# Kernel optimization log

Hardware: AMD Instinct MI355X
Metric: run time of the kernel (lower is better)

The kernel has to match this reference:

```python
import jax, jax.numpy as jnp
import numpy as np

N, E, IN_C, HID_C, OUT_C = 50000, 800000, 64, 64, 8
NEG_SLOPE = 0.2


def setup_inputs() -> dict:
    key = jax.random.key(0)
    ks = jax.random.split(key, 12)
    return {
        "x": jax.random.normal(ks[0], (N, IN_C), dtype=jnp.float32),
        "edge_index": jax.random.randint(ks[1], (2, E), 0, N, dtype=jnp.int64),
        "edge_value": jax.random.uniform(ks[2], (E,), dtype=jnp.float32),
        "W1": jax.random.normal(ks[3], (IN_C, HID_C), dtype=jnp.float32) * 0.1,
        "a1_src": jax.random.normal(ks[4], (HID_C,), dtype=jnp.float32) * 0.1,
        "a1_dst": jax.random.normal(ks[5], (HID_C,), dtype=jnp.float32) * 0.1,
        "b1": jnp.zeros((HID_C,), dtype=jnp.float32),
        "W2": jax.random.normal(ks[6], (HID_C, OUT_C), dtype=jnp.float32) * 0.1,
        "a2_src": jax.random.normal(ks[7], (OUT_C,), dtype=jnp.float32) * 0.1,
        "a2_dst": jax.random.normal(ks[8], (OUT_C,), dtype=jnp.float32) * 0.1,
        "b2": jnp.zeros((OUT_C,), dtype=jnp.float32),
    }


def _rgat_conv(x, src, dst, edge_value, W, a_src, a_dst, b, n_nodes):
    # Linear transform: [N, out_c]
    h = x @ W
    # Per-node attention halves, gathered per edge -> per-edge logit
    e_src = h @ a_src  # [N]
    e_dst = h @ a_dst  # [N]
    logits = jax.nn.leaky_relu(e_src[src] + e_dst[dst], negative_slope=NEG_SLOPE)  # [E]
    # Segment softmax over destination neighborhoods (numerically stable)
    m = jax.ops.segment_max(logits, dst, num_segments=n_nodes)  # [N]
    ex = jnp.exp(logits - m[dst])
    denom = jax.ops.segment_sum(ex, dst, num_segments=n_nodes)  # [N]
    alpha = ex / (denom[dst] + 1e-16)  # [E]
    # Edge-weighted messages, scatter-aggregate to destinations
    msg = (alpha * edge_value)[:, None] * h[src]  # [E, out_c]
    out = jax.ops.segment_sum(msg, dst, num_segments=n_nodes)  # [N, out_c]
    return out + b


def reference(x, edge_index, edge_value, W1, a1_src, a1_dst, b1, W2, a2_src, a2_dst, b2):
    src, dst = edge_index[0], edge_index[1]
    n = x.shape[0]
    hid = _rgat_conv(x, src, dst, edge_value, W1, a1_src, a1_dst, b1, n)
    hid = jax.nn.relu(hid)
    out = _rgat_conv(hid, src, dst, edge_value, W2, a2_src, a2_dst, b2, n)
    return jax.nn.log_softmax(out, axis=1)
```

## Files before the change

### kernel.cpp

```cpp
#include <hip/hip_runtime.h>
#include <hip/hip_fp16.h>
#include <math.h>


#define CHUNK 4096
#define NBKT  256
#define CAP   6144

typedef unsigned long long ull;
typedef float v2f __attribute__((ext_vector_type(2)));

struct PartSmem {
    int lhist[NBKT], lbase[NBKT], lcur[NBKT], gbase[NBKT];
    ull buf[CHUNK];
};
struct GemmSmem {
    float4 Wl[64 * 16];
    float  Xt[64 * 64];
};
union FusedSmem { PartSmem p; GemmSmem g; };


__global__ void __launch_bounds__(256) part_gemm_kernel(
    const int* __restrict__ src, const int* __restrict__ dst,
    const float* __restrict__ ev, int* __restrict__ bcnt,
    ull* __restrict__ ped, int E, int nchunks,
    const float* __restrict__ x, const float* __restrict__ W,
    const float* __restrict__ a_src, const float* __restrict__ a_dst,
    unsigned* __restrict__ h, float* __restrict__ es, float* __restrict__ ed,
    int N)
{
    __shared__ FusedSmem sm;
    const int t = threadIdx.x;

    if (blockIdx.x < nchunks) {
        int e0 = blockIdx.x * CHUNK;
        int cnt = min(CHUNK, E - e0);
        sm.p.lhist[t] = 0;
        __syncthreads();
        for (int i = t; i < cnt; i += 256)
            atomicAdd(&sm.p.lhist[dst[e0 + i] >> 8], 1);
        __syncthreads();
        int myc = sm.p.lhist[t];
        sm.p.lbase[t] = myc;
        __syncthreads();
        for (int o = 1; o < 256; o <<= 1) {
            int add = (t >= o) ? sm.p.lbase[t - o] : 0;
            __syncthreads();
            sm.p.lbase[t] += add;
            __syncthreads();
        }
        int excl = sm.p.lbase[t] - myc;
        sm.p.gbase[t] = myc ? atomicAdd(&bcnt[t], myc) : 0;
        __syncthreads();
        sm.p.lbase[t] = excl;
        sm.p.lcur[t] = excl;
        __syncthreads();
        for (int i = t; i < cnt; i += 256) {
            int e = e0 + i;
            int d = dst[e];
            int b = d >> 8;
            unsigned p = (unsigned)src[e] | ((unsigned)(d & 255) << 16)
                       | ((unsigned)b << 24);
            ull q = (ull)p | ((ull)__float_as_uint(ev[e]) << 32);
            int r = atomicAdd(&sm.p.lcur[b], 1);
            sm.p.buf[r] = q;
        }
        __syncthreads();
        for (int i = t; i < cnt; i += 256) {
            ull q = sm.p.buf[i];
            int b = (int)((q >> 24) & 255);
            ped[(size_t)b * CAP + sm.p.gbase[b] + i - sm.p.lbase[b]] = q;
        }
        return;
    }

    const int n0 = (blockIdx.x - nchunks) * 64;

    #pragma unroll
    for (int i = 0; i < 4; ++i)
        sm.g.Wl[t + i * 256] = ((const float4*)W)[t + i * 256];

    #pragma unroll
    for (int i = 0; i < 4; ++i) {
        int f   = t + i * 256;
        int row = f >> 4, kq = f & 15;
        int grow = n0 + row;
        float4 v = make_float4(0.f, 0.f, 0.f, 0.f);
        if (grow < N) v = ((const float4*)x)[(size_t)grow * 16 + kq];
        int rs = row ^ ((kq & 3) << 2);
        sm.g.Xt[(kq * 4 + 0) * 64 + rs] = v.x;
        sm.g.Xt[(kq * 4 + 1) * 64 + rs] = v.y;
        sm.g.Xt[(kq * 4 + 2) * 64 + rs] = v.z;
        sm.g.Xt[(kq * 4 + 3) * 64 + rs] = v.w;
    }

    const int tx = t & 15;
    const int ty = t >> 4;
    const float4 asv = ((const float4*)a_src)[tx];
    const float4 adv = ((const float4*)a_dst)[tx];
    __syncthreads();

    float4 acc0 = make_float4(0.f,0.f,0.f,0.f);
    float4 acc1 = make_float4(0.f,0.f,0.f,0.f);
    float4 acc2 = make_float4(0.f,0.f,0.f,0.f);
    float4 acc3 = make_float4(0.f,0.f,0.f,0.f);

    #pragma unroll 8
    for (int k = 0; k < 64; ++k) {
        int swz = (k >> 2) & 3;
        const float4 xr = *(const float4*)&sm.g.Xt[k * 64 + ((ty ^ swz) << 2)];
        const float4 wv = sm.g.Wl[k * 16 + tx];
        acc0.x += xr.x * wv.x; acc0.y += xr.x * wv.y;
        acc0.z += xr.x * wv.z; acc0.w += xr.x * wv.w;
        acc1.x += xr.y * wv.x; acc1.y += xr.y * wv.y;
        acc1.z += xr.y * wv.z; acc1.w += xr.y * wv.w;
        acc2.x += xr.z * wv.x; acc2.y += xr.z * wv.y;
        acc2.z += xr.z * wv.z; acc2.w += xr.z * wv.w;
        acc3.x += xr.w * wv.x; acc3.y += xr.w * wv.y;
        acc3.z += xr.w * wv.z; acc3.w += xr.w * wv.w;
    }

    float4 accs[4] = {acc0, acc1, acc2, acc3};
    #pragma unroll
    for (int r = 0; r < 4; ++r) {
        int grow = n0 + ty * 4 + r;
        float4 a = accs[r];
        if (grow < N) {
            int lo = __builtin_amdgcn_cvt_pk_fp8_f32(a.x, a.y, 0, false);
            int pk = __builtin_amdgcn_cvt_pk_fp8_f32(a.z, a.w, lo, true);
            h[(size_t)grow * 16 + tx] = (unsigned)pk;
        }
        float ps = a.x * asv.x + a.y * asv.y + a.z * asv.z + a.w * asv.w;
        float pd = a.x * adv.x + a.y * adv.y + a.z * adv.z + a.w * adv.w;
        #pragma unroll
        for (int o = 8; o > 0; o >>= 1) {
            ps += __shfl_xor(ps, o);
            pd += __shfl_xor(pd, o);
        }
        if (tx == 0 && grow < N) { es[grow] = ps; ed[grow] = pd; }
    }
}


__global__ void __launch_bounds__(1024) csrw_agg64_kernel(
    const ull* __restrict__ ped, const int* __restrict__ bcnt,
    const float* __restrict__ es1, const float* __restrict__ ed1,
    int* __restrict__ off, int* __restrict__ deg, ull* __restrict__ csre,
    const unsigned* __restrict__ h1, const float* __restrict__ b1,
    const float* __restrict__ W2, const float* __restrict__ a2s,
    const float* __restrict__ a2d, float* __restrict__ h2,
    float* __restrict__ es2, float* __restrict__ ed2, int N)
{
    __shared__ int    lhist[256], lbase[256], lcur[256], degl[256];
    __shared__ float  den1[256], eds[256];
    __shared__ float  W2s[64 * 8];
    __shared__ float  w1v[CAP];
    __shared__ unsigned short svl[CAP];

    const int b = blockIdx.x, t = threadIdx.x;
    const int cnt = min(bcnt[b], CAP);
    const size_t base = (size_t)b * CAP;

    if (t < 256) {
        const int nodeT = b * 256 + t;
        lhist[t] = 0;
        den1[t] = 0.f;
        eds[t] = (nodeT < N) ? ed1[nodeT] : 0.f;
    }
    if (t < 128) ((float4*)W2s)[t] = ((const float4*)W2)[t];
    __syncthreads();

    for (int i = t; i < cnt; i += 1024)
        atomicAdd(&lhist[(int)((ped[base + i] >> 16) & 255)], 1);
    __syncthreads();
    int myc = (t < 256) ? lhist[t] : 0;
    if (t < 256) lbase[t] = myc;
    __syncthreads();
    for (int o = 1; o < 256; o <<= 1) {
        int add = (t >= o && t < 256) ? lbase[t - o] : 0;
        __syncthreads();
        if (t < 256) lbase[t] += add;
        __syncthreads();
    }
    if (t < 256) {
        const int excl = lbase[t] - myc;
        const int nodeT = b * 256 + t;
        lcur[t] = excl;
        degl[t] = myc;
        if (nodeT < N) { off[nodeT] = (int)base + excl; deg[nodeT] = myc; }
    }
    __syncthreads();
    if (t < 256) lbase[t] -= myc;
    __syncthreads();

    for (int i = t; i < cnt; i += 1024) {
        const ull q = ped[base + i];
        const int sv   = (int)(q & 0xFFFFull);
        const int dloc = (int)((q >> 16) & 255);
        const float evv = __uint_as_float((unsigned)(q >> 32));
        float z = es1[sv] + eds[dloc];
        float l = z > 0.f ? z : 0.2f * z;
        float e = __expf(l);
        atomicAdd(&den1[dloc], e);
        const int pos = atomicAdd(&lcur[dloc], 1);
        w1v[pos] = e * evv;
        svl[pos] = (unsigned short)sv;
        csre[base + pos] = (q & 0xFFFFFFFF00000000ull)
                         | ((ull)(unsigned)(dloc << 16)) | (ull)(unsigned)sv;
    }
    __syncthreads();

    const int wid = t >> 6, lane = t & 63;
    const int grp = lane >> 2, sl = lane & 3;
    const int nloc = wid * 16 + grp;
    const int n = b * 256 + nloc;
    if (n >= N) return;

    const int dg   = degl[nloc];
    const int lbeg = lbase[nloc];

    float acc[16];
    #pragma unroll
    for (int k = 0; k < 16; ++k) acc[k] = 0.f;

    for (int j0 = 0; j0 < dg; j0 += 4) {
        #pragma unroll
        for (int ts = 0; ts < 4; ++ts) {
            const int jj  = j0 + ts;
            const int idx = lbeg + min(jj, dg - 1);
            const int svt = (int)svl[idx];
            float wt = w1v[idx];
            wt = (jj < dg) ? wt : 0.f;
            const uint4 u = *(const uint4*)&h1[(size_t)svt * 16 + sl * 4];
            v2f fa = __builtin_amdgcn_cvt_pk_f32_fp8((int)u.x, false);
            v2f fb = __builtin_amdgcn_cvt_pk_f32_fp8((int)u.x, true);
            v2f fc = __builtin_amdgcn_cvt_pk_f32_fp8((int)u.y, false);
            v2f fd = __builtin_amdgcn_cvt_pk_f32_fp8((int)u.y, true);
            v2f fe = __builtin_amdgcn_cvt_pk_f32_fp8((int)u.z, false);
            v2f ff = __builtin_amdgcn_cvt_pk_f32_fp8((int)u.z, true);
            v2f fg = __builtin_amdgcn_cvt_pk_f32_fp8((int)u.w, false);
            v2f fh = __builtin_amdgcn_cvt_pk_f32_fp8((int)u.w, true);
            acc[0]  += wt * fa.x; acc[1]  += wt * fa.y;
            acc[2]  += wt * fb.x; acc[3]  += wt * fb.y;
            acc[4]  += wt * fc.x; acc[5]  += wt * fc.y;
            acc[6]  += wt * fd.x; acc[7]  += wt * fd.y;
            acc[8]  += wt * fe.x; acc[9]  += wt * fe.y;
            acc[10] += wt * ff.x; acc[11] += wt * ff.y;
            acc[12] += wt * fg.x; acc[13] += wt * fg.y;
            acc[14] += wt * fh.x; acc[15] += wt * fh.y;
        }
    }

    const float inv = 1.f / (den1[nloc] + 1e-16f);

    const float4 b1v0 = *(const float4*)&b1[sl * 16];
    const float4 b1v1 = *(const float4*)&b1[sl * 16 + 4];
    const float4 b1v2 = *(const float4*)&b1[sl * 16 + 8];
    const float4 b1v3 = *(const float4*)&b1[sl * 16 + 12];

    float hid[16];
    hid[0]  = fmaxf(acc[0]  * inv + b1v0.x, 0.f);
    hid[1]  = fmaxf(acc[1]  * inv + b1v0.y, 0.f);
    hid[2]  = fmaxf(acc[2]  * inv + b1v0.z, 0.f);
    hid[3]  = fmaxf(acc[3]  * inv + b1v0.w, 0.f);
    hid[4]  = fmaxf(acc[4]  * inv + b1v1.x, 0.f);
    hid[5]  = fmaxf(acc[5]  * inv + b1v1.y, 0.f);
    hid[6]  = fmaxf(acc[6]  * inv + b1v1.z, 0.f);
    hid[7]  = fmaxf(acc[7]  * inv + b1v1.w, 0.f);
    hid[8]  = fmaxf(acc[8]  * inv + b1v2.x, 0.f);
    hid[9]  = fmaxf(acc[9]  * inv + b1v2.y, 0.f);
    hid[10] = fmaxf(acc[10] * inv + b1v2.z, 0.f);
    hid[11] = fmaxf(acc[11] * inv + b1v2.w, 0.f);
    hid[12] = fmaxf(acc[12] * inv + b1v3.x, 0.f);
    hid[13] = fmaxf(acc[13] * inv + b1v3.y, 0.f);
    hid[14] = fmaxf(acc[14] * inv + b1v3.z, 0.f);
    hid[15] = fmaxf(acc[15] * inv + b1v3.w, 0.f);

    float p[8];
    #pragma unroll
    for (int o = 0; o < 8; ++o) p[o] = 0.f;
    #pragma unroll
    for (int k = 0; k < 16; ++k) {
        const float4 wA = *(const float4*)&W2s[(sl * 16 + k) * 8];
        const float4 wB = *(const float4*)&W2s[(sl * 16 + k) * 8 + 4];
        p[0] += hid[k] * wA.x; p[1] += hid[k] * wA.y;
        p[2] += hid[k] * wA.z; p[3] += hid[k] * wA.w;
        p[4] += hid[k] * wB.x; p[5] += hid[k] * wB.y;
        p[6] += hid[k] * wB.z; p[7] += hid[k] * wB.w;
    }
    float s4[4];
    {
        const bool hi = (sl & 1);
        #pragma unroll
        for (int k = 0; k < 4; ++k) {
            float keep = hi ? p[k + 4] : p[k];
            float send = hi ? p[k]     : p[k + 4];
            s4[k] = keep + __shfl_xor(send, 1);
        }
    }
    float s2[2];
    {
        const bool hi = (sl & 2);
        #pragma unroll
        for (int k = 0; k < 2; ++k) {
            float keep = hi ? s4[k + 2] : s4[k];
            float send = hi ? s4[k]     : s4[k + 2];
            s2[k] = keep + __shfl_xor(send, 2);
        }
    }
    const int oo = 4 * (sl & 1) + 2 * ((sl >> 1) & 1);

    float tsv = s2[0] * a2s[oo] + s2[1] * a2s[oo + 1];
    float tdv = s2[0] * a2d[oo] + s2[1] * a2d[oo + 1];
    tsv += __shfl_xor(tsv, 1); tdv += __shfl_xor(tdv, 1);
    tsv += __shfl_xor(tsv, 2); tdv += __shfl_xor(tdv, 2);

    *(float2*)&h2[(size_t)n * 8 + oo] = make_float2(s2[0], s2[1]);
    if (sl == 0) { es2[n] = tsv; ed2[n] = tdv; }
}


__global__ void __launch_bounds__(1024) agg8_lsm_kernel(
    const int* __restrict__ bcnt, const int* __restrict__ off,
    const int* __restrict__ deg, const ull* __restrict__ csre,
    const float* __restrict__ es2, const float* __restrict__ ed2,
    const float* __restrict__ h2, const float* __restrict__ b2,
    float* __restrict__ out, int N)
{
    __shared__ float w2v[CAP];
    __shared__ unsigned short svl[CAP];
    __shared__ float den2[256], ed2s[256];

    const int b = blockIdx.x, t = threadIdx.x;
    const int cnt = min(bcnt[b], CAP);
    const size_t base = (size_t)b * CAP;

    if (t < 256) {
        const int nodeT = b * 256 + t;
        den2[t] = 0.f;
        ed2s[t] = (nodeT < N) ? ed2[nodeT] : 0.f;
    }
    __syncthreads();

    for (int i = t; i < cnt; i += 1024) {
        const ull r = csre[base + i];
        const int sv   = (int)(r & 0xFFFFull);
        const int dloc = (int)((r >> 16) & 255);
        const float evv = __uint_as_float((unsigned)(r >> 32));
        float z = es2[sv] + ed2s[dloc];
        float l = z > 0.f ? z : 0.2f * z;
        float q = __expf(l);
        atomicAdd(&den2[dloc], q);
        w2v[i] = q * evv;
        svl[i] = (unsigned short)sv;
    }
    __syncthreads();

    const int wid = t >> 6, lane = t & 63;
    const int grp = lane >> 2, sl = lane & 3;
    const int nloc = wid * 16 + grp;
    const int n = b * 256 + nloc;
    if (n >= N) return;

    const int dg   = deg[n];
    const int lbeg = off[n] - (int)base;

    float a0 = 0.f, a1 = 0.f;

    for (int j0 = 0; j0 < dg; j0 += 4) {
        #pragma unroll
        for (int ts = 0; ts < 4; ++ts) {
            const int jj  = j0 + ts;
            const int idx = lbeg + min(jj, dg - 1);
            const int svt = (int)svl[idx];
            float wt = w2v[idx];
            wt = (jj < dg) ? wt : 0.f;
            const float2 f = *(const float2*)&h2[(size_t)svt * 8 + 2 * sl];
            a0 += wt * f.x;
            a1 += wt * f.y;
        }
    }

    const float inv = 1.f / (den2[nloc] + 1e-16f);
    float v0 = a0 * inv + b2[2 * sl];
    float v1 = a1 * inv + b2[2 * sl + 1];

    float vm = fmaxf(v0, v1);
    vm = fmaxf(vm, __shfl_xor(vm, 1));
    vm = fmaxf(vm, __shfl_xor(vm, 2));
    float s = __expf(v0 - vm) + __expf(v1 - vm);
    s += __shfl_xor(s, 1);
    s += __shfl_xor(s, 2);
    float lse = vm + logf(s);
    *(float2*)&out[(size_t)n * 8 + 2 * sl] = make_float2(v0 - lse, v1 - lse);
}


extern "C" void kernel_launch(void* const* d_in, const int* in_sizes, int n_in,
                              void* d_out, int out_size, void* d_ws, size_t ws_size,
                              hipStream_t stream)
{
    const float* x   = (const float*)d_in[0];
    const int*   ei  = (const int*)d_in[1];
    const float* ev  = (const float*)d_in[2];
    const float* W1  = (const float*)d_in[3];
    const float* a1s = (const float*)d_in[4];
    const float* a1d = (const float*)d_in[5];
    const float* b1  = (const float*)d_in[6];
    const float* W2  = (const float*)d_in[7];
    const float* a2s = (const float*)d_in[8];
    const float* a2d = (const float*)d_in[9];
    const float* b2  = (const float*)d_in[10];
    float* out = (float*)d_out;

    const int N = in_sizes[0] / 64;
    const int E = in_sizes[2];
    const int* srcp = ei;
    const int* dstp = ei + E;
    const int nchunks = (E + CHUNK - 1) / CHUNK;
    const int ngemm   = (N + 63) / 64;
    const int nbuck   = (N + 255) / 256;

    ull*   ped  = (ull*)d_ws;
    ull*   csre = ped + (size_t)NBKT * CAP;
    int*   bcnt = (int*)(csre + (size_t)NBKT * CAP);
    int*   off  = bcnt + NBKT;
    int*   deg  = off + N;
    float* es1  = (float*)(deg + N);
    float* ed1  = es1 + N;
    float* es2  = ed1 + N;
    float* ed2  = es2 + N;
    unsigned* h1 = (unsigned*)(ed2 + N);
    float* h2   = (float*)(h1 + (size_t)N * 16);

    hipMemsetAsync(bcnt, 0, NBKT * sizeof(int), stream);

    part_gemm_kernel<<<nchunks + ngemm, 256, 0, stream>>>(
        srcp, dstp, ev, bcnt, ped, E, nchunks,
        x, W1, a1s, a1d, h1, es1, ed1, N);

    csrw_agg64_kernel<<<nbuck, 1024, 0, stream>>>(
        ped, bcnt, es1, ed1, off, deg, csre,
        h1, b1, W2, a2s, a2d, h2, es2, ed2, N);

    agg8_lsm_kernel<<<nbuck, 1024, 0, stream>>>(
        bcnt, off, deg, csre, es2, ed2, h2, b2, out, N);
}
```

Before: 137.9 us.

## Fuse layer-1 aggregation and layer-2 aggregation via grid-wide atomic barrier

Merges the layer-1 CSR/aggregate kernel and the layer-2 aggregate/log-softmax kernel into one persistent launch. Per-bucket edge data (source, local destination, edge value) stays in shared memory across a software grid barrier, so the csre/off/deg global arrays are no longer written and reread. It also removes one kernel launch. The cost is extra shared memory per block and a spin barrier that assumes all 196 blocks are co-resident, which risks deadlock if they are not.

New measurement: 147.7 us. +7.2%, slower.

```diff
diff --git a/kernel.cpp b/kernel.cpp
--- a/kernel.cpp
+++ b/kernel.cpp
@@ -9,6 +9,8 @@
 
 typedef unsigned long long ull;
 typedef float v2f __attribute__((ext_vector_type(2)));
+
+union F2U { float2 f; ull u; };
 
 struct PartSmem {
     int lhist[NBKT], lbase[NBKT], lcur[NBKT], gbase[NBKT];
@@ -143,20 +145,22 @@
 }
 
 
-__global__ void __launch_bounds__(1024) csrw_agg64_kernel(
+__global__ void __launch_bounds__(1024) fused_l12_kernel(
     const ull* __restrict__ ped, const int* __restrict__ bcnt,
     const float* __restrict__ es1, const float* __restrict__ ed1,
-    int* __restrict__ off, int* __restrict__ deg, ull* __restrict__ csre,
     const unsigned* __restrict__ h1, const float* __restrict__ b1,
     const float* __restrict__ W2, const float* __restrict__ a2s,
     const float* __restrict__ a2d, float* __restrict__ h2,
-    float* __restrict__ es2, float* __restrict__ ed2, int N)
+    float* __restrict__ es2, const float* __restrict__ b2,
+    float* __restrict__ out, int N, int nbuck, int* __restrict__ barrier_ctr)
 {
     __shared__ int    lhist[256], lbase[256], lcur[256], degl[256];
-    __shared__ float  den1[256], eds[256];
+    __shared__ float  den[256], eds[256];
     __shared__ float  W2s[64 * 8];
-    __shared__ float  w1v[CAP];
+    __shared__ float  wv[CAP];
+    __shared__ float  evl[CAP];
     __shared__ unsigned short svl[CAP];
+    __shared__ unsigned char  dlocl[CAP];
 
     const int b = blockIdx.x, t = threadIdx.x;
     const int cnt = min(bcnt[b], CAP);
@@ -165,7 +169,7 @@
     if (t < 256) {
         const int nodeT = b * 256 + t;
         lhist[t] = 0;
-        den1[t] = 0.f;
+        den[t] = 0.f;
         eds[t] = (nodeT < N) ? ed1[nodeT] : 0.f;
     }
     if (t < 128) ((float4*)W2s)[t] = ((const float4*)W2)[t];
@@ -184,11 +188,8 @@
         __syncthreads();
     }
     if (t < 256) {
-        const int excl = lbase[t] - myc;
-        const int nodeT = b * 256 + t;
-        lcur[t] = excl;
+        lcur[t] = lbase[t] - myc;
         degl[t] = myc;
-        if (nodeT < N) { off[nodeT] = (int)base + excl; deg[nodeT] = myc; }
     }
     __syncthreads();
     if (t < 256) lbase[t] -= myc;
@@ -202,12 +203,12 @@
         float z = es1[sv] + eds[dloc];
         float l = z > 0.f ? z : 0.2f * z;
         float e = __expf(l);
-        atomicAdd(&den1[dloc], e);
+        atomicAdd(&den[dloc], e);
         const int pos = atomicAdd(&lcur[dloc], 1);
-        w1v[pos] = e * evv;
-        svl[pos] = (unsigned short)sv;
-        csre[base + pos] = (q & 0xFFFFFFFF00000000ull)
-                         | ((ull)(unsigned)(dloc << 16)) | (ull)(unsigned)sv;
+        wv[pos]    = e * evv;
+        svl[pos]   = (unsigned short)sv;
+        dlocl[pos] = (unsigned char)dloc;
+        evl[pos]   = evv;
     }
     __syncthreads();
 
@@ -215,185 +216,178 @@
     const int grp = lane >> 2, sl = lane & 3;
     const int nloc = wid * 16 + grp;
     const int n = b * 256 + nloc;
-    if (n >= N) return;
-
-    const int dg   = degl[nloc];
-    const int lbeg = lbase[nloc];
-
-    float acc[16];
-    #pragma unroll
-    for (int k = 0; k < 16; ++k) acc[k] = 0.f;
-
-    for (int j0 = 0; j0 < dg; j0 += 4) {
+
+    if (n < N) {
+        const int dg   = degl[nloc];
+        const int lbeg = lbase[nloc];
+
+        float acc[16];
         #pragma unroll
-        for (int ts = 0; ts < 4; ++ts) {
-            const int jj  = j0 + ts;
-            const int idx = lbeg + min(jj, dg - 1);
-            const int svt = (int)svl[idx];
-            float wt = w1v[idx];
-            wt = (jj < dg) ? wt : 0.f;
-            const uint4 u = *(const uint4*)&h1[(size_t)svt * 16 + sl * 4];
-            v2f fa = __builtin_amdgcn_cvt_pk_f32_fp8((int)u.x, false);
-            v2f fb = __builtin_amdgcn_cvt_pk_f32_fp8((int)u.x, true);
-            v2f fc = __builtin_amdgcn_cvt_pk_f32_fp8((int)u.y, false);
-            v2f fd = __builtin_amdgcn_cvt_pk_f32_fp8((int)u.y, true);
-            v2f fe = __builtin_amdgcn_cvt_pk_f32_fp8((int)u.z, false);
-            v2f ff = __builtin_amdgcn_cvt_pk_f32_fp8((int)u.z, true);
-            v2f fg = __builtin_amdgcn_cvt_pk_f32_fp8((int)u.w, false);
-            v2f fh = __builtin_amdgcn_cvt_pk_f32_fp8((int)u.w, true);
-            acc[0]  += wt * fa.x; acc[1]  += wt * fa.y;
-            acc[2]  += wt * fb.x; acc[3]  += wt * fb.y;
-            acc[4]  += wt * fc.x; acc[5]  += wt * fc.y;
-            acc[6]  += wt * fd.x; acc[7]  += wt * fd.y;
-            acc[8]  += wt * fe.x; acc[9]  += wt * fe.y;
-            acc[10] += wt * ff.x; acc[11] += wt * ff.y;
-            acc[12] += wt * fg.x; acc[13] += wt * fg.y;
-            acc[14] += wt * fh.x; acc[15] += wt * fh.y;
-        }
-    }
-
-    const float inv = 1.f / (den1[nloc] + 1e-16f);
-
-    const float4 b1v0 = *(const float4*)&b1[sl * 16];
-    const float4 b1v1 = *(const float4*)&b1[sl * 16 + 4];
-    const float4 b1v2 = *(const float4*)&b1[sl * 16 + 8];
-    const float4 b1v3 = *(const float4*)&b1[sl * 16 + 12];
-
-    float hid[16];
-    hid[0]  = fmaxf(acc[0]  * inv + b1v0.x, 0.f);
-    hid[1]  = fmaxf(acc[1]  * inv + b1v0.y, 0.f);
-    hid[2]  = fmaxf(acc[2]  * inv + b1v0.z, 0.f);
-    hid[3]  = fmaxf(acc[3]  * inv + b1v0.w, 0.f);
-    hid[4]  = fmaxf(acc[4]  * inv + b1v1.x, 0.f);
-    hid[5]  = fmaxf(acc[5]  * inv + b1v1.y, 0.f);
-    hid[6]  = fmaxf(acc[6]  * inv + b1v1.z, 0.f);
-    hid[7]  = fmaxf(acc[7]  * inv + b1v1.w, 0.f);
-    hid[8]  = fmaxf(acc[8]  * inv + b1v2.x, 0.f);
-    hid[9]  = fmaxf(acc[9]  * inv + b1v2.y, 0.f);
-    hid[10] = fmaxf(acc[10] * inv + b1v2.z, 0.f);
-    hid[11] = fmaxf(acc[11] * inv + b1v2.w, 0.f);
-    hid[12] = fmaxf(acc[12] * inv + b1v3.x, 0.f);
-    hid[13] = fmaxf(acc[13] * inv + b1v3.y, 0.f);
-    hid[14] = fmaxf(acc[14] * inv + b1v3.z, 0.f);
-    hid[15] = fmaxf(acc[15] * inv + b1v3.w, 0.f);
-
-    float p[8];
-    #pragma unroll
-    for (int o = 0; o < 8; ++o) p[o] = 0.f;
-    #pragma unroll
-    for (int k = 0; k < 16; ++k) {
-        const float4 wA = *(const float4*)&W2s[(sl * 16 + k) * 8];
-        const float4 wB = *(const float4*)&W2s[(sl * 16 + k) * 8 + 4];
-        p[0] += hid[k] * wA.x; p[1] += hid[k] * wA.y;
-        p[2] += hid[k] * wA.z; p[3] += hid[k] * wA.w;
-        p[4] += hid[k] * wB.x; p[5] += hid[k] * wB.y;
-        p[6] += hid[k] * wB.z; p[7] += hid[k] * wB.w;
-    }
-    float s4[4];
-    {
-        const bool hi = (sl & 1);
+        for (int k = 0; k < 16; ++k) acc[k] = 0.f;
+
+        for (int j0 = 0; j0 < dg; j0 += 4) {
+            #pragma unroll
+            for (int ts = 0; ts < 4; ++ts) {
+                const int jj  = j0 + ts;
+                const int idx = lbeg + min(jj, dg - 1);
+                const int svt = (int)svl[idx];
+                float wt = wv[idx];
+                wt = (jj < dg) ? wt : 0.f;
+                const uint4 u = *(const uint4*)&h1[(size_t)svt * 16 + sl * 4];
+                v2f fa = __builtin_amdgcn_cvt_pk_f32_fp8((int)u.x, false);
+                v2f fb = __builtin_amdgcn_cvt_pk_f32_fp8((int)u.x, true);
+                v2f fc = __builtin_amdgcn_cvt_pk_f32_fp8((int)u.y, false);
+                v2f fd = __builtin_amdgcn_cvt_pk_f32_fp8((int)u.y, true);
+                v2f fe = __builtin_amdgcn_cvt_pk_f32_fp8((int)u.z, false);
+                v2f ff = __builtin_amdgcn_cvt_pk_f32_fp8((int)u.z, true);
+                v2f fg = __builtin_amdgcn_cvt_pk_f32_fp8((int)u.w, false);
+                v2f fh = __builtin_amdgcn_cvt_pk_f32_fp8((int)u.w, true);
+                acc[0]  += wt * fa.x; acc[1]  += wt * fa.y;
+                acc[2]  += wt * fb.x; acc[3]  += wt * fb.y;
+                acc[4]  += wt * fc.x; acc[5]  += wt * fc.y;
+                acc[6]  += wt * fd.x; acc[7]  += wt * fd.y;
+                acc[8]  += wt * fe.x; acc[9]  += wt * fe.y;
+                acc[10] += wt * ff.x; acc[11] += wt * ff.y;
+                acc[12] += wt * fg.x; acc[13] += wt * fg.y;
+                acc[14] += wt * fh.x; acc[15] += wt * fh.y;
+            }
+        }
+
+        const float inv = 1.f / (den[nloc] + 1e-16f);
+
+        const float4 b1v0 = *(const float4*)&b1[sl * 16];
+        const float4 b1v1 = *(const float4*)&b1[sl * 16 + 4];
+        const float4 b1v2 = *(const float4*)&b1[sl * 16 + 8];
+        const float4 b1v3 = *(const float4*)&b1[sl * 16 + 12];
+
+        float hid[16];
+        hid[0]  = fmaxf(acc[0]  * inv + b1v0.x, 0.f);
+        hid[1]  = fmaxf(acc[1]  * inv + b1v0.y, 0.f);
+        hid[2]  = fmaxf(acc[2]  * inv + b1v0.z, 0.f);
+        hid[3]  = fmaxf(acc[3]  * inv + b1v0.w, 0.f);
+        hid[4]  = fmaxf(acc[4]  * inv + b1v1.x, 0.f);
+        hid[5]  = fmaxf(acc[5]  * inv + b1v1.y, 0.f);
+        hid[6]  = fmaxf(acc[6]  * inv + b1v1.z, 0.f);
+        hid[7]  = fmaxf(acc[7]  * inv + b1v1.w, 0.f);
+        hid[8]  = fmaxf(acc[8]  * inv + b1v2.x, 0.f);
+        hid[9]  = fmaxf(acc[9]  * inv + b1v2.y, 0.f);
+        hid[10] = fmaxf(acc[10] * inv + b1v2.z, 0.f);
+        hid[11] = fmaxf(acc[11] * inv + b1v2.w, 0.f);
+        hid[12] = fmaxf(acc[12] * inv + b1v3.x, 0.f);
+        hid[13] = fmaxf(acc[13] * inv + b1v3.y, 0.f);
+        hid[14] = fmaxf(acc[14] * inv + b1v3.z, 0.f);
+        hid[15] = fmaxf(acc[15] * inv + b1v3.w, 0.f);
+
+        float p[8];
         #pragma unroll
-        for (int k = 0; k < 4; ++k) {
-            float keep = hi ? p[k + 4] : p[k];
-            float send = hi ? p[k]     : p[k + 4];
-            s4[k] = keep + __shfl_xor(send, 1);
-        }
-    }
-    float s2[2];
-    {
-        const bool hi = (sl & 2);
+        for (int o = 0; o < 8; ++o) p[o] = 0.f;
         #pragma unroll
-        for (int k = 0; k < 2; ++k) {
-            float keep = hi ? s4[k + 2] : s4[k];
-            float send = hi ? s4[k]     : s4[k + 2];
-            s2[k] = keep + __shfl_xor(send, 2);
-        }
-    }
-    const int oo = 4 * (sl & 1) + 2 * ((sl >> 1) & 1);
-
-    float tsv = s2[0] * a2s[oo] + s2[1] * a2s[oo + 1];
-    float tdv = s2[0] * a2d[oo] + s2[1] * a2d[oo + 1];
-    tsv += __shfl_xor(tsv, 1); tdv += __shfl_xor(tdv, 1);
-    tsv += __shfl_xor(tsv, 2); tdv += __shfl_xor(tdv, 2);
-
-    *(float2*)&h2[(size_t)n * 8 + oo] = make_float2(s2[0], s2[1]);
-    if (sl == 0) { es2[n] = tsv; ed2[n] = tdv; }
-}
-
-
-__global__ void __launch_bounds__(1024) agg8_lsm_kernel(
-    const int* __restrict__ bcnt, const int* __restrict__ off,
-    const int* __restrict__ deg, const ull* __restrict__ csre,
-    const float* __restrict__ es2, const float* __restrict__ ed2,
-    const float* __restrict__ h2, const float* __restrict__ b2,
-    float* __restrict__ out, int N)
-{
-    __shared__ float w2v[CAP];
-    __shared__ unsigned short svl[CAP];
-    __shared__ float den2[256], ed2s[256];
-
-    const int b = blockIdx.x, t = threadIdx.x;
-    const int cnt = min(bcnt[b], CAP);
-    const size_t base = (size_t)b * CAP;
-
-    if (t < 256) {
-        const int nodeT = b * 256 + t;
-        den2[t] = 0.f;
-        ed2s[t] = (nodeT < N) ? ed2[nodeT] : 0.f;
-    }
-    __syncthreads();
-
+        for (int k = 0; k < 16; ++k) {
+            const float4 wA = *(const float4*)&W2s[(sl * 16 + k) * 8];
+            const float4 wB = *(const float4*)&W2s[(sl * 16 + k) * 8 + 4];
+            p[0] += hid[k] * wA.x; p[1] += hid[k] * wA.y;
+            p[2] += hid[k] * wA.z; p[3] += hid[k] * wA.w;
+            p[4] += hid[k] * wB.x; p[5] += hid[k] * wB.y;
+            p[6] += hid[k] * wB.z; p[7] += hid[k] * wB.w;
+        }
+        float s4[4];
+        {
+            const bool hi = (sl & 1);
+            #pragma unroll
+            for (int k = 0; k < 4; ++k) {
+                float keep = hi ? p[k + 4] : p[k];
+                float send = hi ? p[k]     : p[k + 4];
+                s4[k] = keep + __shfl_xor(send, 1);
+            }
+        }
+        float s2[2];
+        {
+            const bool hi = (sl & 2);
+            #pragma unroll
+            for (int k = 0; k < 2; ++k) {
+                float keep = hi ? s4[k + 2] : s4[k];
+                float send = hi ? s4[k]     : s4[k + 2];
+                s2[k] = keep + __shfl_xor(send, 2);
+            }
+        }
+        const int oo = 4 * (sl & 1) + 2 * ((sl >> 1) & 1);
+
+        float tsv = s2[0] * a2s[oo] + s2[1] * a2s[oo + 1];
+        float tdv = s2[0] * a2d[oo] + s2[1] * a2d[oo + 1];
+        tsv += __shfl_xor(tsv, 1); tdv += __shfl_xor(tdv, 1);
+        tsv += __shfl_xor(tsv, 2); tdv += __shfl_xor(tdv, 2);
+
+        F2U hv; hv.f = make_float2(s2[0], s2[1]);
+        __hip_atomic_store((ull*)&h2[(size_t)n * 8 + oo], hv.u,
+                           __ATOMIC_RELAXED, __HIP_MEMORY_SCOPE_AGENT);
+        if (sl == 0) {
+            __hip_atomic_store(&es2[n], tsv,
+                               __ATOMIC_RELAXED, __HIP_MEMORY_SCOPE_AGENT);
+            eds[nloc] = tdv;
+        }
+    }
+    __syncthreads();
+
+    if (t == 0) {
+        __threadfence();
+        atomicAdd(barrier_ctr, 1);
+        while (__hip_atomic_load(barrier_ctr, __ATOMIC_ACQUIRE,
+                                 __HIP_MEMORY_SCOPE_AGENT) < nbuck)
+            __builtin_amdgcn_s_sleep(8);
+    }
+    __syncthreads();
+
+    if (t < 256) den[t] = 0.f;
+    __syncthreads();
     for (int i = t; i < cnt; i += 1024) {
-        const ull r = csre[base + i];
-        const int sv   = (int)(r & 0xFFFFull);
-        const int dloc = (int)((r >> 16) & 255);
-        const float evv = __uint_as_float((unsigned)(r >> 32));
-        float z = es2[sv] + ed2s[dloc];
+        const int sv = (int)svl[i];
+        const int dl = (int)dlocl[i];
+        const float es2v = __hip_atomic_load(&es2[sv], __ATOMIC_RELAXED,
+                                             __HIP_MEMORY_SCOPE_AGENT);
+        float z = es2v + eds[dl];
         float l = z > 0.f ? z : 0.2f * z;
         float q = __expf(l);
-        atomicAdd(&den2[dloc], q);
-        w2v[i] = q * evv;
-        svl[i] = (unsigned short)sv;
-    }
-    __syncthreads();
-
-    const int wid = t >> 6, lane = t & 63;
-    const int grp = lane >> 2, sl = lane & 3;
-    const int nloc = wid * 16 + grp;
-    const int n = b * 256 + nloc;
-    if (n >= N) return;
-
-    const int dg   = deg[n];
-    const int lbeg = off[n] - (int)base;
-
-    float a0 = 0.f, a1 = 0.f;
-
-    for (int j0 = 0; j0 < dg; j0 += 4) {
-        #pragma unroll
-        for (int ts = 0; ts < 4; ++ts) {
-            const int jj  = j0 + ts;
-            const int idx = lbeg + min(jj, dg - 1);
-            const int svt = (int)svl[idx];
-            float wt = w2v[idx];
-            wt = (jj < dg) ? wt : 0.f;
-            const float2 f = *(const float2*)&h2[(size_t)svt * 8 + 2 * sl];
-            a0 += wt * f.x;
-            a1 += wt * f.y;
-        }
-    }
-
-    const float inv = 1.f / (den2[nloc] + 1e-16f);
-    float v0 = a0 * inv + b2[2 * sl];
-    float v1 = a1 * inv + b2[2 * sl + 1];
-
-    float vm = fmaxf(v0, v1);
-    vm = fmaxf(vm, __shfl_xor(vm, 1));
-    vm = fmaxf(vm, __shfl_xor(vm, 2));
-    float s = __expf(v0 - vm) + __expf(v1 - vm);
-    s += __shfl_xor(s, 1);
-    s += __shfl_xor(s, 2);
-    float lse = vm + logf(s);
-    *(float2*)&out[(size_t)n * 8 + 2 * sl] = make_float2(v0 - lse, v1 - lse);
+        atomicAdd(&den[dl], q);
+        wv[i] = q * evl[i];
+    }
+    __syncthreads();
+
+    if (n < N) {
+        const int dg   = degl[nloc];
+        const int lbeg = lbase[nloc];
+
+        float a0 = 0.f, a1 = 0.f;
+
+        for (int j0 = 0; j0 < dg; j0 += 4) {
+            #pragma unroll
+            for (int ts = 0; ts < 4; ++ts) {
+                const int jj  = j0 + ts;
+                const int idx = lbeg + min(jj, dg - 1);
+                const int svt = (int)svl[idx];
+                float wt = wv[idx];
+                wt = (jj < dg) ? wt : 0.f;
+                F2U hv;
+                hv.u = __hip_atomic_load(
+                    (const ull*)&h2[(size_t)svt * 8 + 2 * sl],
+                    __ATOMIC_RELAXED, __HIP_MEMORY_SCOPE_AGENT);
+                a0 += wt * hv.f.x;
+                a1 += wt * hv.f.y;
+            }
+        }
+
+        const float inv = 1.f / (den[nloc] + 1e-16f);
+        float v0 = a0 * inv + b2[2 * sl];
+        float v1 = a1 * inv + b2[2 * sl + 1];
+
+        float vm = fmaxf(v0, v1);
+        vm = fmaxf(vm, __shfl_xor(vm, 1));
+        vm = fmaxf(vm, __shfl_xor(vm, 2));
+        float s = __expf(v0 - vm) + __expf(v1 - vm);
+        s += __shfl_xor(s, 1);
+        s += __shfl_xor(s, 2);
+        float lse = vm + logf(s);
+        *(float2*)&out[(size_t)n * 8 + 2 * sl] = make_float2(v0 - lse, v1 - lse);
+    }
 }
 
 
@@ -423,27 +417,21 @@
     const int nbuck   = (N + 255) / 256;
 
     ull*   ped  = (ull*)d_ws;
-    ull*   csre = ped + (size_t)NBKT * CAP;
-    int*   bcnt = (int*)(csre + (size_t)NBKT * CAP);
-    int*   off  = bcnt + NBKT;
-    int*   deg  = off + N;
-    float* es1  = (float*)(deg + N);
+    int*   bcnt = (int*)(ped + (size_t)NBKT * CAP);
+    int*   bctr = bcnt + NBKT;
+    float* es1  = (float*)(bctr + 64);
     float* ed1  = es1 + N;
     float* es2  = ed1 + N;
-    float* ed2  = es2 + N;
-    unsigned* h1 = (unsigned*)(ed2 + N);
+    unsigned* h1 = (unsigned*)(es2 + N);
     float* h2   = (float*)(h1 + (size_t)N * 16);
 
-    hipMemsetAsync(bcnt, 0, NBKT * sizeof(int), stream);
+    hipMemsetAsync(bcnt, 0, (NBKT + 64) * sizeof(int), stream);
 
     part_gemm_kernel<<<nchunks + ngemm, 256, 0, stream>>>(
         srcp, dstp, ev, bcnt, ped, E, nchunks,
         x, W1, a1s, a1d, h1, es1, ed1, N);
 
-    csrw_agg64_kernel<<<nbuck, 1024, 0, stream>>>(
-        ped, bcnt, es1, ed1, off, deg, csre,
-        h1, b1, W2, a2s, a2d, h2, es2, ed2, N);
-
-    agg8_lsm_kernel<<<nbuck, 1024, 0, stream>>>(
-        bcnt, off, deg, csre, es2, ed2, h2, b2, out, N);
+    fused_l12_kernel<<<nbuck, 1024, 0, stream>>>(
+        ped, bcnt, es1, ed1, h1, b1, W2, a2s, a2d,
+        h2, es2, b2, out, N, nbuck, bctr);
 }
```
